# Kernel tuning notes

Measured on AMD Instinct MI355X. Metric: run time of the kernel, lower is better.

Reference implementation:

```python
import jax, jax.numpy as jnp
import numpy as np

BS, P, D, C, ND, K, NC, H = 32, 196, 512, 100, 51, 50, 800, 8
LAMBDA, BETA, EPS = 0.5, 5.5, 1e-5


def _ln(x, g, b):
    m = x.mean(-1, keepdims=True)
    v = jnp.mean((x - m) ** 2, axis=-1, keepdims=True)
    return (x - m) / jnp.sqrt(v + EPS) * g + b


def _norm(x):
    return x / jnp.linalg.norm(x, axis=-1, keepdims=True)


def _bonder(x, kv, Wq, Wk, Wv, Wo, ln1_g, ln1_b, ln2_g, ln2_b, W1, b1, W2, b2):
    # cross-attn block: queries = text prompts [B,N,d], kv = retrieved patch feats [B,M,d]
    B, N, d = x.shape
    M = kv.shape[1]
    dh = d // H
    q = (_ln(x, ln1_g, ln1_b) @ Wq).reshape(B, N, H, dh)
    k = (kv @ Wk).reshape(B, M, H, dh)
    v = (kv @ Wv).reshape(B, M, H, dh)
    att = jax.nn.softmax(jnp.einsum('bnhd,bmhd->bhnm', q, k) / np.sqrt(dh).astype(np.float32), axis=-1)
    o = jnp.einsum('bhnm,bmhd->bnhd', att, v).reshape(B, N, d) @ Wo
    x = x + o
    h = _ln(x, ln2_g, ln2_b)
    return x + jax.nn.gelu(h @ W1 + b1) @ W2 + b2


def _dense_logits(gfeat, local, all_text, mean_text, topk):
    # gfeat [b,d], local [b,p,d], all_text [C,n,d], mean_text [C,d]
    base = gfeat @ mean_text.T                                   # [b,C]
    w = jnp.einsum('bd,bpd->bp', gfeat, local)                   # [b,p]
    atf = jnp.transpose(all_text, (1, 0, 2))                     # [n,C,d]
    v = jax.nn.softmax(jnp.einsum('cd,ncd->nc', mean_text, atf), axis=0)  # [n,C]
    sim = jnp.einsum('bpd,ncd->bcpn', local, atf)                # [b,C,p,n]
    vals, idx = jax.lax.top_k(jnp.transpose(sim, (0, 1, 3, 2)), topk)     # over patch dim
    sim_topk = jnp.transpose(vals, (0, 1, 3, 2))                 # [b,C,k,n]
    idx = jnp.transpose(idx, (0, 1, 3, 2))                       # [b,C,k,n]
    idx_w = idx[:, 0, :, 0]                                      # [b,k]
    w_topk = jax.nn.softmax(jnp.take_along_axis(w, idx_w, axis=1), axis=-1)  # [b,k]
    weight = jnp.einsum('bk,nc->bckn', w_topk, v)                # [b,C,k,n]
    return base + jnp.sum(sim_topk * weight, axis=(-2, -1))


def setup_inputs() -> dict:
    key = jax.random.key(0)
    ks = jax.random.split(key, 12)
    s = 0.02
    labels = jax.random.randint(ks[10], (BS,), 0, C)
    cache_labels = jax.random.randint(ks[11], (NC,), 0, C)
    return {
        'local_feat': jax.random.normal(ks[0], (BS, P, D)),
        'Wa': jnp.eye(D) + s * jax.random.normal(ks[1], (D, D)),
        'text_cache': jax.random.normal(ks[2], (C, ND, D)),
        'Wq': s * jax.random.normal(ks[3], (D, D)),
        'Wk': s * jax.random.normal(ks[4], (D, D)),
        'Wv': s * jax.random.normal(ks[5], (D, D)),
        'Wo': s * jax.random.normal(ks[6], (D, D)),
        'ln1_g': jnp.ones((D,)), 'ln1_b': jnp.zeros((D,)),
        'ln2_g': jnp.ones((D,)), 'ln2_b': jnp.zeros((D,)),
        'W1': s * jax.random.normal(ks[7], (D, 4 * D)), 'b1': jnp.zeros((4 * D,)),
        'W2': s * jax.random.normal(ks[8], (4 * D, D)), 'b2': jnp.zeros((D,)),
        'logit_scale': jnp.asarray(np.log(1.0 / 0.07), jnp.float32),
        'ensemble_scale': jnp.asarray(-2.0, jnp.float32),
        'raw_cache_local_feats': jax.random.normal(ks[9], (NC, P, D)),
        'cache_values': jax.nn.one_hot(cache_labels, C, dtype=jnp.float32),
        'labels': labels,
        'cache_labels': cache_labels,
    }


def reference(local_feat, Wa, text_cache, Wq, Wk, Wv, Wo, ln1_g, ln1_b, ln2_g, ln2_b,
              W1, b1, W2, b2, logit_scale, ensemble_scale, raw_cache_local_feats,
              cache_values, labels, cache_labels):
    bs = local_feat.shape[0]
    adapted_local = _norm(local_feat @ Wa.T)                      # [b,p,d]
    adapted_global = _norm(adapted_local.mean(axis=1))            # [b,d]
    base_text_mean = _norm(jax.lax.stop_gradient(text_cache).mean(axis=1))  # [C,d]
    sim_to_text = jax.lax.stop_gradient(adapted_local @ base_text_mean.T)   # [b,p,C]
    sim_target = sim_to_text[jnp.arange(bs), :, labels]           # [b,p]
    topk_idx = jax.lax.top_k(sim_target, K)[1]
    botk_idx = jax.lax.top_k(-sim_target, K)[1]
    topk_feats = jnp.take_along_axis(adapted_local, topk_idx[:, :, None], axis=1)  # [b,K,d]
    botk_feats = jnp.take_along_axis(adapted_local, botk_idx[:, :, None], axis=1)
    # training branch: bonder on ground-truth class prompts, scatter into bias_full
    l2p = text_cache[labels]                                      # [b,ND,d]
    text_bias = _bonder(l2p, jax.lax.stop_gradient(topk_feats),
                        Wq, Wk, Wv, Wo, ln1_g, ln1_b, ln2_g, ln2_b, W1, b1, W2, b2)
    bias_full = jnp.zeros((bs, C, ND, D), local_feat.dtype).at[jnp.arange(bs), labels].set(text_bias)
    bias_avg = bias_full.mean(axis=0)                             # [C,ND,d]
    refined = text_cache + LAMBDA * bias_avg
    refined_norm = _norm(refined)
    refined_mean_norm = _norm(refined_norm.mean(axis=1))
    ls = jnp.exp(logit_scale)
    inter = ls * _dense_logits(adapted_global, adapted_local, refined_norm, refined_mean_norm, K)
    # tip-adapter cache branch
    cache_adapted = _norm(raw_cache_local_feats @ Wa.T)           # [Nc,p,d]
    cache_sim = jax.lax.stop_gradient(cache_adapted @ base_text_mean.T)
    cache_sim_target = cache_sim[jnp.arange(cache_sim.shape[0]), :, cache_labels]
    cache_topk_idx = jax.lax.top_k(cache_sim_target, K)[1]
    cache_topk_feats = jnp.take_along_axis(cache_adapted, cache_topk_idx[:, :, None], axis=1)
    cache_keys = _norm(cache_topk_feats.mean(axis=1))             # [Nc,d]
    query_keys = _norm(topk_feats.mean(axis=1))                   # [b,d]
    affinity = jnp.exp(-BETA * (1.0 - query_keys @ cache_keys.T))
    intra = affinity @ cache_values                               # [b,C]
    scale = jax.nn.sigmoid(ensemble_scale)
    logits = inter * (1 - scale) + intra * ls * scale
    return (logits, inter, intra, adapted_global, topk_feats, botk_feats, refined_norm)
```

## Files before the change

kernel.cpp:

```cpp
#include <hip/hip_runtime.h>
#include <math.h>

#define DEV static __device__ __forceinline__

typedef __attribute__((ext_vector_type(8))) short short8v;
typedef __attribute__((ext_vector_type(8))) _Float16 half8v;
typedef __attribute__((ext_vector_type(4))) float f32x4;

DEV unsigned encf(float f){ unsigned b=__float_as_uint(f); return b ^ (0x80000000u | (unsigned)((int)b>>31)); }
DEV unsigned long long pkvi(float v, int idx){
  return ((unsigned long long)encf(v)<<32) | (unsigned long long)(0xffffffffu - (unsigned)idx);
}
DEV unsigned long long wave_max_ull(unsigned long long u){
  #pragma unroll
  for (int m=1;m<64;m<<=1){ unsigned long long o = __shfl_xor(u, m); if (o>u) u=o; }
  return u;
}
DEV float wave_sum(float v){
  #pragma unroll
  for (int m=32;m;m>>=1) v += __shfl_xor(v, m);
  return v;
}
DEV float blk_sum256(float v, float* scr){
  v = wave_sum(v);
  __syncthreads();
  if ((threadIdx.x & 63)==0) scr[threadIdx.x>>6] = v;
  __syncthreads();
  return scr[0]+scr[1]+scr[2]+scr[3];
}
DEV float gelu_f(float x){ return 0.5f*x*(1.f + tanhf(0.7978845608028654f*(x + 0.044715f*x*x*x))); }
DEV unsigned short f2bf(float x){
  unsigned u = __float_as_uint(x);
  unsigned r = (u + 0x7fffu + ((u>>16)&1u)) >> 16;
  return (unsigned short)r;
}
DEV float bf2f(unsigned short h){ return __uint_as_float(((unsigned)h)<<16); }
DEV void gld16(const void* g, void* l){
  __builtin_amdgcn_global_load_lds((const __attribute__((address_space(1))) unsigned int*)g,
                                   (__attribute__((address_space(3))) unsigned int*)l, 16, 0, 0);
}
template<int CTRL>
DEV float dppf(float x){
  return __int_as_float(__builtin_amdgcn_mov_dpp(__float_as_int(x), CTRL, 0xF, 0xF, false));
}

template<bool TRANS, bool SUBI>
__global__ __launch_bounds__(256) void k_convw(const float* __restrict__ W,
    unsigned short* __restrict__ hi, unsigned short* __restrict__ lo, int R, int C){
  int n = blockIdx.x;
  int K = TRANS ? R : C;
  for (int k = threadIdx.x; k < K; k += 256){
    float x = TRANS ? W[(size_t)k*C + n] : W[(size_t)n*C + k];
    if (SUBI && k==n) x -= 1.f;
    unsigned short h = f2bf(x);
    hi[(size_t)n*K + k] = h;
    if (lo) lo[(size_t)n*K + k] = f2bf(x - bf2f(h));
  }
}

__global__ __launch_bounds__(256) void k_convw4(
  const float* __restrict__ Wq, const float* __restrict__ Wk,
  const float* __restrict__ Wv, const float* __restrict__ Wo,
  unsigned short* __restrict__ qh, unsigned short* __restrict__ ql,
  unsigned short* __restrict__ kh, unsigned short* __restrict__ kl,
  unsigned short* __restrict__ vh, unsigned short* __restrict__ vl,
  unsigned short* __restrict__ oh, unsigned short* __restrict__ ol)
{
  int n = blockIdx.x;
  const float* W; unsigned short *hi, *lo;
  switch(blockIdx.y){
    case 0: W=Wq; hi=qh; lo=ql; break;
    case 1: W=Wk; hi=kh; lo=kl; break;
    case 2: W=Wv; hi=vh; lo=vl; break;
    default: W=Wo; hi=oh; lo=ol; break;
  }
  for (int k = threadIdx.x; k < 512; k += 256){
    float x = W[(size_t)k*512 + n];
    unsigned short h = f2bf(x);
    hi[(size_t)n*512 + k] = h;
    lo[(size_t)n*512 + k] = f2bf(x - bf2f(h));
  }
}

__global__ __launch_bounds__(256) void k_convd2(const float* __restrict__ Wa, unsigned short* __restrict__ Dfrag){
  int e = blockIdx.x;
  int tile = e>>4, lr = e&15;
  for (int d = threadIdx.x; d < 512; d += 256){
    float x = Wa[(size_t)e*512 + d] - (e==d ? 1.f : 0.f);
    union { _Float16 hh; unsigned short u; } cv;
    cv.hh = (_Float16)x;
    int ks = d>>5, q = (d>>3)&3, el = d&7;
    Dfrag[(size_t)(((tile*16+ks)*64 + q*16 + lr)*8 + el)] = cv.u;
  }
}

template<int EPI>
__global__ __launch_bounds__(256,2) void gemmAB(
  const unsigned short* __restrict__ Ahi, const unsigned short* __restrict__ Alo,
  const unsigned short* __restrict__ Bhi, const unsigned short* __restrict__ Blo,
  float* __restrict__ Cp, unsigned short* __restrict__ Chi, unsigned short* __restrict__ Clo,
  const int M, const int N, const int K,
  const float* __restrict__ bias, const float* __restrict__ resid)
{
  __shared__ __align__(16) char sm[32768];
  const int t = threadIdx.x, lane = t&63, wid = t>>6;
  const int row0 = blockIdx.x*128, col0 = blockIdx.y*128;
  f32x4 acc[2][8];
  #pragma unroll
  for (int i=0;i<2;++i)
    #pragma unroll
    for (int j=0;j<8;++j) acc[i][j] = (f32x4){0.f,0.f,0.f,0.f};

  int offA[2], offB[8];
  #pragma unroll
  for (int mt=0; mt<2; ++mt){
    int row = (2*wid+mt)*16 + (lane&15);
    int sp = (lane>>4) ^ ((row>>1)&3);
    offA[mt] = row*64 + sp*16;
  }
  #pragma unroll
  for (int nt=0; nt<8; ++nt){
    int row = nt*16 + (lane&15);
    int sp = (lane>>4) ^ ((row>>1)&3);
    offB[nt] = row*64 + sp*16;
  }

  const int nks = K >> 5;
  for (int ks=0; ks<nks; ++ks){
    #pragma unroll
    for (int i=0;i<2;++i){
      int s = i*256 + t, row = s>>2, sl2 = s&3, slog = sl2 ^ ((row>>1)&3);
      size_t ga = (size_t)(row0+row)*K + ks*32 + slog*8;
      size_t gb = (size_t)(col0+row)*K + ks*32 + slog*8;
      int dst = (i*256 + wid*64)*16;
      gld16(Ahi + ga, sm + dst);
      gld16(Alo + ga, sm + 8192 + dst);
      gld16(Bhi + gb, sm + 16384 + dst);
      gld16(Blo + gb, sm + 24576 + dst);
    }
    __syncthreads();
    short8v ah0 = *(short8v*)(sm + offA[0]);
    short8v ah1 = *(short8v*)(sm + offA[1]);
    short8v al0 = *(short8v*)(sm + 8192 + offA[0]);
    short8v al1 = *(short8v*)(sm + 8192 + offA[1]);
    #pragma unroll
    for (int nt=0; nt<8; ++nt){
      short8v bh = *(short8v*)(sm + 16384 + offB[nt]);
      short8v bl = *(short8v*)(sm + 24576 + offB[nt]);
      acc[0][nt] = __builtin_amdgcn_mfma_f32_16x16x32_bf16(ah0, bh, acc[0][nt], 0,0,0);
      acc[0][nt] = __builtin_amdgcn_mfma_f32_16x16x32_bf16(ah0, bl, acc[0][nt], 0,0,0);
      acc[0][nt] = __builtin_amdgcn_mfma_f32_16x16x32_bf16(al0, bh, acc[0][nt], 0,0,0);
      acc[1][nt] = __builtin_amdgcn_mfma_f32_16x16x32_bf16(ah1, bh, acc[1][nt], 0,0,0);
      acc[1][nt] = __builtin_amdgcn_mfma_f32_16x16x32_bf16(ah1, bl, acc[1][nt], 0,0,0);
      acc[1][nt] = __builtin_amdgcn_mfma_f32_16x16x32_bf16(al1, bh, acc[1][nt], 0,0,0);
    }
    __syncthreads();
  }

  #pragma unroll
  for (int mt=0; mt<2; ++mt){
    #pragma unroll
    for (int nt=0; nt<8; ++nt){
      int n = col0 + nt*16 + (lane&15);
      int mb = row0 + (2*wid+mt)*16 + (lane>>4)*4;
      #pragma unroll
      for (int j=0;j<4;++j){
        int m = mb + j;
        if (m < M){
          float v = acc[mt][nt][j];
          if (EPI & 1) v += bias[n];
          if (EPI & 2) v = gelu_f(v);
          if (EPI & 4) v += resid[(size_t)m*N + n];
          if (EPI & 8){
            unsigned short h = f2bf(v);
            Chi[(size_t)m*N + n] = h;
            Clo[(size_t)m*N + n] = f2bf(v - bf2f(h));
          } else {
            Cp[(size_t)m*N + n] = v;
          }
        }
      }
    }
  }
}

__global__ __launch_bounds__(256,2) void gemmABQKV(
  const unsigned short* __restrict__ lnH, const unsigned short* __restrict__ lnL,
  const unsigned short* __restrict__ tkH, const unsigned short* __restrict__ tkL,
  const unsigned short* __restrict__ qh, const unsigned short* __restrict__ ql,
  const unsigned short* __restrict__ kh, const unsigned short* __restrict__ kl,
  const unsigned short* __restrict__ vh, const unsigned short* __restrict__ vl,
  float* __restrict__ qb, float* __restrict__ kb, float* __restrict__ vbuf)
{
  __shared__ __align__(16) char sm[32768];
  const int z = blockIdx.z;
  const unsigned short* Ahi = (z==0)? lnH : tkH;
  const unsigned short* Alo = (z==0)? lnL : tkL;
  const unsigned short* Bhi = (z==0)? qh : (z==1? kh : vh);
  const unsigned short* Blo = (z==0)? ql : (z==1? kl : vl);
  float* Cp = (z==0)? qb : (z==1? kb : vbuf);
  const int M = (z==0)? 1632 : 1600;
  const int K = 512, N = 512;
  const int t = threadIdx.x, lane = t&63, wid = t>>6;
  const int row0 = blockIdx.x*128, col0 = blockIdx.y*128;
  f32x4 acc[2][8];
  #pragma unroll
  for (int i=0;i<2;++i)
    #pragma unroll
    for (int j=0;j<8;++j) acc[i][j] = (f32x4){0.f,0.f,0.f,0.f};

  int offA[2], offB[8];
  #pragma unroll
  for (int mt=0; mt<2; ++mt){
    int row = (2*wid+mt)*16 + (lane&15);
    int sp = (lane>>4) ^ ((row>>1)&3);
    offA[mt] = row*64 + sp*16;
  }
  #pragma unroll
  for (int nt=0; nt<8; ++nt){
    int row = nt*16 + (lane&15);
    int sp = (lane>>4) ^ ((row>>1)&3);
    offB[nt] = row*64 + sp*16;
  }

  for (int ks=0; ks<16; ++ks){
    #pragma unroll
    for (int i=0;i<2;++i){
      int s = i*256 + t, row = s>>2, sl2 = s&3, slog = sl2 ^ ((row>>1)&3);
      size_t ga = (size_t)(row0+row)*K + ks*32 + slog*8;
      size_t gb = (size_t)(col0+row)*K + ks*32 + slog*8;
      int dst = (i*256 + wid*64)*16;
      gld16(Ahi + ga, sm + dst);
      gld16(Alo + ga, sm + 8192 + dst);
      gld16(Bhi + gb, sm + 16384 + dst);
      gld16(Blo + gb, sm + 24576 + dst);
    }
    __syncthreads();
    short8v ah0 = *(short8v*)(sm + offA[0]);
    short8v ah1 = *(short8v*)(sm + offA[1]);
    short8v al0 = *(short8v*)(sm + 8192 + offA[0]);
    short8v al1 = *(short8v*)(sm + 8192 + offA[1]);
    #pragma unroll
    for (int nt=0; nt<8; ++nt){
      short8v bh = *(short8v*)(sm + 16384 + offB[nt]);
      short8v bl = *(short8v*)(sm + 24576 + offB[nt]);
      acc[0][nt] = __builtin_amdgcn_mfma_f32_16x16x32_bf16(ah0, bh, acc[0][nt], 0,0,0);
      acc[0][nt] = __builtin_amdgcn_mfma_f32_16x16x32_bf16(ah0, bl, acc[0][nt], 0,0,0);
      acc[0][nt] = __builtin_amdgcn_mfma_f32_16x16x32_bf16(al0, bh, acc[0][nt], 0,0,0);
      acc[1][nt] = __builtin_amdgcn_mfma_f32_16x16x32_bf16(ah1, bh, acc[1][nt], 0,0,0);
      acc[1][nt] = __builtin_amdgcn_mfma_f32_16x16x32_bf16(ah1, bl, acc[1][nt], 0,0,0);
      acc[1][nt] = __builtin_amdgcn_mfma_f32_16x16x32_bf16(al1, bh, acc[1][nt], 0,0,0);
    }
    __syncthreads();
  }

  #pragma unroll
  for (int mt=0; mt<2; ++mt){
    #pragma unroll
    for (int nt=0; nt<8; ++nt){
      int n = col0 + nt*16 + (lane&15);
      int mb = row0 + (2*wid+mt)*16 + (lane>>4)*4;
      #pragma unroll
      for (int j=0;j<4;++j){
        int m = mb + j;
        if (m < M) Cp[(size_t)m*N + n] = acc[mt][nt][j];
      }
    }
  }
}

__global__ __launch_bounds__(512,1) void k_un7(
  const float* __restrict__ raw, const unsigned short* __restrict__ Dfrag,
  const float* __restrict__ zm, const int* __restrict__ clab,
  float* __restrict__ cdot, float* __restrict__ norm2)
{
  __shared__ __align__(16) char Alds[131072];
  __shared__ float n2sq[128];
  __shared__ float n2x[4][128];
  const int t = threadIdx.x, lane = t&63;
  const int wid = t>>6, wm = wid>>2, wn = wid&3;
  const int m0 = blockIdx.x*128;

  {
    const int row = t>>2, sl = t&3;
    const int slg = sl ^ ((row>>1)&3);
    const float* rp = raw + ((size_t)(m0+row))*512 + slg*8;
    const float* zp = zm + (size_t)clab[(m0+row)/196]*512 + slg*8;
    float sq=0.f, cd=0.f;
    #pragma unroll
    for (int c4=0; c4<4; ++c4){
      float4 pr[8], pz[8];
      #pragma unroll
      for (int i=0;i<4;++i){
        pr[2*i]   = *(const float4*)(rp + (c4*4+i)*32);
        pr[2*i+1] = *(const float4*)(rp + (c4*4+i)*32 + 4);
      }
      #pragma unroll
      for (int i=0;i<4;++i){
        pz[2*i]   = *(const float4*)(zp + (c4*4+i)*32);
        pz[2*i+1] = *(const float4*)(zp + (c4*4+i)*32 + 4);
      }
      #pragma unroll
      for (int i=0;i<4;++i){
        int ks = c4*4+i;
        float xs[8] = {pr[2*i].x,pr[2*i].y,pr[2*i].z,pr[2*i].w,
                       pr[2*i+1].x,pr[2*i+1].y,pr[2*i+1].z,pr[2*i+1].w};
        float zs[8] = {pz[2*i].x,pz[2*i].y,pz[2*i].z,pz[2*i].w,
                       pz[2*i+1].x,pz[2*i+1].y,pz[2*i+1].z,pz[2*i+1].w};
        union { _Float16 h[8]; f32x4 f; } uh;
        #pragma unroll
        for (int u=0;u<8;++u){
          uh.h[u] = (_Float16)xs[u];
          sq = fmaf(xs[u],xs[u],sq);
          cd = fmaf(xs[u],zs[u],cd);
        }
        *(f32x4*)(Alds + ks*8192 + t*16) = uh.f;
      }
    }
    sq += __shfl_xor(sq,1); sq += __shfl_xor(sq,2);
    cd += __shfl_xor(cd,1); cd += __shfl_xor(cd,2);
    if (sl==0){ n2sq[row] = sq; cdot[m0+row] = cd; }
  }
  __syncthreads();

  int offA[4];
  #pragma unroll
  for (int mt=0; mt<4; ++mt){
    int row = wm*64 + mt*16 + (lane&15);
    int sp = (lane>>4) ^ ((row>>1)&3);
    offA[mt] = row*64 + sp*16;
  }
  const half8v* Dv = (const half8v*)Dfrag;

  float pacc[4][4];
  #pragma unroll
  for (int a_=0;a_<4;++a_)
    #pragma unroll
    for (int b_=0;b_<4;++b_) pacc[a_][b_]=0.f;

  for (int eb2=0; eb2<4; ++eb2){
    f32x4 acc[4][2];
    #pragma unroll
    for (int a_=0;a_<4;++a_)
      #pragma unroll
      for (int b_=0;b_<2;++b_) acc[a_][b_] = (f32x4){0.f,0.f,0.f,0.f};

    #pragma unroll 4
    for (int ks=0; ks<16; ++ks){
      half8v af[4], bf[2];
      #pragma unroll
      for (int mt=0; mt<4; ++mt) af[mt] = *(half8v*)(Alds + ks*8192 + offA[mt]);
      #pragma unroll
      for (int nt=0; nt<2; ++nt) bf[nt] = Dv[(size_t)(((eb2*8 + wn*2 + nt)*16 + ks)*64 + lane)];
      #pragma unroll
      for (int mt=0; mt<4; ++mt)
        #pragma unroll
        for (int nt=0; nt<2; ++nt)
          acc[mt][nt] = __builtin_amdgcn_mfma_f32_16x16x32_f16(af[mt], bf[nt], acc[mt][nt], 0,0,0);
    }

    #pragma unroll
    for (int mt=0; mt<4; ++mt){
      #pragma unroll
      for (int j=0;j<4;++j){
        int row = wm*64 + mt*16 + (lane>>4)*4 + j;
        float p = 0.f;
        #pragma unroll
        for (int nt=0; nt<2; ++nt){
          float U = acc[mt][nt][j];
          int eg = eb2*128 + wn*32 + nt*16 + (lane&15);
          int kse = eg>>5, o = eg&31;
          int sll = (o>>3) ^ ((row>>1)&3);
          float rh = (float)*(const _Float16*)(Alds + kse*8192 + row*64 + sll*16 + (o&7)*2);
          p = fmaf(U, 2.f*rh + U, p);
        }
        p += __shfl_xor(p,1); p += __shfl_xor(p,2); p += __shfl_xor(p,4); p += __shfl_xor(p,8);
        pacc[mt][j] += p;
      }
    }
  }

  __syncthreads();
  if ((lane&15)==0){
    #pragma unroll
    for (int mt=0; mt<4; ++mt)
      #pragma unroll
      for (int j=0;j<4;++j)
        n2x[wn][wm*64 + mt*16 + (lane>>4)*4 + j] = pacc[mt][j];
  }
  __syncthreads();
  if (t < 128)
    norm2[m0+t] = n2sq[t] + n2x[0][t] + n2x[1][t] + n2x[2][t] + n2x[3][t];
}

__global__ __launch_bounds__(256) void k_rownorm(const float* __restrict__ in, float* __restrict__ out,
                                                 unsigned short* __restrict__ bfo, int nrows){
  __shared__ float scr[4];
  int r = blockIdx.x, t = threadIdx.x; (void)nrows;
  const float* p = in + (size_t)r*512;
  float x0 = p[t], x1 = p[t+256];
  float ss = blk_sum256(x0*x0 + x1*x1, scr);
  float inv = 1.f/sqrtf(ss);
  float v0 = x0*inv, v1 = x1*inv;
  out[(size_t)r*512 + t] = v0;
  out[(size_t)r*512 + t + 256] = v1;
  if (bfo){
    size_t br = (size_t)(r/196)*256 + (r%196);
    bfo[br*512 + t]     = f2bf(v0);
    bfo[br*512 + t+256] = f2bf(v1);
  }
}

__global__ __launch_bounds__(256) void k_meanrows_norm(const float* __restrict__ in, int nper,
                                                       float* __restrict__ o1, float* __restrict__ o2){
  __shared__ float scr[4];
  int g = blockIdx.x, t = threadIdx.x;
  float s0=0.f, s1=0.f;
  const float* bp = in + (size_t)g*nper*512;
  for (int r=0;r<nper;++r){ s0 += bp[(size_t)r*512+t]; s1 += bp[(size_t)r*512+t+256]; }
  float ss = blk_sum256(s0*s0+s1*s1, scr);
  float inv = 1.f/sqrtf(ss);
  float v0 = s0*inv, v1 = s1*inv;
  o1[(size_t)g*512+t]=v0; o1[(size_t)g*512+t+256]=v1;
  if (o2){ o2[(size_t)g*512+t]=v0; o2[(size_t)g*512+t+256]=v1; }
}

__global__ __launch_bounds__(256) void k_zmat(const float* __restrict__ btm, const float* __restrict__ Wa, float* __restrict__ z){
  int c = blockIdx.x, t = threadIdx.x;
  float a0=0.f, a1=0.f;
  for (int d=0; d<512; ++d){
    float bv = btm[c*512+d];
    a0 = fmaf(bv, Wa[(size_t)d*512+t], a0);
    a1 = fmaf(bv, Wa[(size_t)d*512+t+256], a1);
  }
  z[c*512+t]=a0; z[c*512+t+256]=a1;
}

__global__ __launch_bounds__(256) void k_dot_bp(const float* __restrict__ AL, const float* __restrict__ vecs,
                                                const int* __restrict__ sel, float* __restrict__ outv, int mode){
  int wid = blockIdx.x*4 + (threadIdx.x>>6);
  int lane = threadIdx.x & 63;
  int b = wid/196;
  int vrow = sel ? sel[b] : (mode ? 0 : b);
  const float* a = AL + (size_t)wid*512 + lane*8;
  const float* v = vecs + (size_t)vrow*512 + lane*8;
  float4 a0 = *(const float4*)a, a1 = *(const float4*)(a+4);
  float4 v0 = *(const float4*)v, v1 = *(const float4*)(v+4);
  float s = a0.x*v0.x + a0.y*v0.y + a0.z*v0.z + a0.w*v0.w
          + a1.x*v1.x + a1.y*v1.y + a1.z*v1.z + a1.w*v1.w;
  s = wave_sum(s);
  if (lane==0) outv[wid] = s;
}

__global__ __launch_bounds__(256) void k_dot2(const float* __restrict__ AL, const float* __restrict__ AGw,
                                              const float* __restrict__ RN00,
                                              float* __restrict__ wbp, float* __restrict__ sLw){
  int wid = blockIdx.x*4 + (threadIdx.x>>6);
  int lane = threadIdx.x & 63;
  int b = wid/196;
  const float* a = AL + (size_t)wid*512 + lane*8;
  const float* v = AGw + (size_t)b*512 + lane*8;
  const float* w = RN00 + lane*8;
  float4 a0=*(const float4*)a, a1=*(const float4*)(a+4);
  float4 v0=*(const float4*)v, v1=*(const float4*)(v+4);
  float4 w0=*(const float4*)w, w1=*(const float4*)(w+4);
  float s1 = a0.x*v0.x+a0.y*v0.y+a0.z*v0.z+a0.w*v0.w + a1.x*v1.x+a1.y*v1.y+a1.z*v1.z+a1.w*v1.w;
  float s2 = a0.x*w0.x+a0.y*w0.y+a0.z*w0.z+a0.w*w0.w + a1.x*w1.x+a1.y*w1.y+a1.z*w1.z+a1.w*w1.w;
  s1 = wave_sum(s1); s2 = wave_sum(s2);
  if (lane==0){ wbp[wid] = s1; sLw[wid] = s2; }
}

__global__ __launch_bounds__(64) void k_topbot(const float* __restrict__ st, int* __restrict__ tki, int* __restrict__ bki){
  int b = blockIdx.x, lane = threadIdx.x;
  float v[4];
  #pragma unroll
  for (int s2=0;s2<4;++s2){ int p = lane + 64*s2; v[s2] = (p<196)? st[b*196+p] : -INFINITY; }
  for (int k=0;k<50;++k){
    unsigned long long best = pkvi(v[0], lane);
    { unsigned long long cc=pkvi(v[1],lane+64);  if(cc>best)best=cc; }
    { unsigned long long cc=pkvi(v[2],lane+128); if(cc>best)best=cc; }
    { unsigned long long cc=pkvi(v[3],lane+192); if(cc>best)best=cc; }
    best = wave_max_ull(best);
    int widx = (int)(0xffffffffu - (unsigned)(best & 0xffffffffu));
    if (lane==0) tki[b*50+k] = widx;
    if ((widx & 63)==lane) v[widx>>6] = -INFINITY;
  }
  #pragma unroll
  for (int s2=0;s2<4;++s2){ int p = lane + 64*s2; v[s2] = (p<196)? -st[b*196+p] : -INFINITY; }
  for (int k=0;k<50;++k){
    unsigned long long best = pkvi(v[0], lane);
    { unsigned long long cc=pkvi(v[1],lane+64);  if(cc>best)best=cc; }
    { unsigned long long cc=pkvi(v[2],lane+128); if(cc>best)best=cc; }
    { unsigned long long cc=pkvi(v[3],lane+192); if(cc>best)best=cc; }
    best = wave_max_ull(best);
    int widx = (int)(0xffffffffu - (unsigned)(best & 0xffffffffu));
    if (lane==0) bki[b*50+k] = widx;
    if ((widx & 63)==lane) v[widx>>6] = -INFINITY;
  }
}

__global__ __launch_bounds__(256) void k_gather_tb(const float* __restrict__ AL, const int* __restrict__ tki, const int* __restrict__ bki,
                                                   float* __restrict__ otk, float* __restrict__ obk, float* __restrict__ qk,
                                                   unsigned short* __restrict__ tkH, unsigned short* __restrict__ tkL){
  __shared__ float scr[4];
  int b = blockIdx.x, t = threadIdx.x;
  float a0=0.f, a1=0.f;
  for (int k=0;k<50;++k){
    int pt = tki[b*50+k];
    const float* rp = AL + ((size_t)b*196+pt)*512;
    float x0 = rp[t], x1 = rp[t+256];
    size_t ro = ((size_t)b*50+k)*512;
    otk[ro + t] = x0; otk[ro + t+256] = x1;
    unsigned short h0 = f2bf(x0), h1 = f2bf(x1);
    tkH[ro + t] = h0;      tkL[ro + t]     = f2bf(x0 - bf2f(h0));
    tkH[ro + t+256] = h1;  tkL[ro + t+256] = f2bf(x1 - bf2f(h1));
    a0 += x0; a1 += x1;
    int pb = bki[b*50+k];
    const float* rb = AL + ((size_t)b*196+pb)*512;
    obk[ro + t] = rb[t]; obk[ro + t+256] = rb[t+256];
  }
  float ss = blk_sum256(a0*a0+a1*a1, scr);
  float inv = 1.f/sqrtf(ss);
  qk[b*512+t] = a0*inv; qk[b*512+t+256] = a1*inv;
}

__global__ __launch_bounds__(256) void k_gxln(const float* __restrict__ tc, const int* __restrict__ labels,
                                              const float* __restrict__ g, const float* __restrict__ be,
                                              float* __restrict__ xb,
                                              unsigned short* __restrict__ hi, unsigned short* __restrict__ lo){
  __shared__ float scr[4];
  int r = blockIdx.x, t = threadIdx.x;
  int b = r/51, n = r%51;
  int lab = labels[b];
  const float* src = tc + ((size_t)lab*51 + n)*512;
  float x0 = src[t], x1 = src[t+256];
  xb[(size_t)r*512+t] = x0; xb[(size_t)r*512+t+256] = x1;
  float s = blk_sum256(x0+x1, scr);
  float mean = s*(1.f/512.f);
  float ss = blk_sum256(x0*x0+x1*x1, scr);
  float var = ss*(1.f/512.f) - mean*mean;
  float inv = 1.f/sqrtf(var + 1e-5f);
  float v0 = (x0-mean)*inv*g[t]     + be[t];
  float v1 = (x1-mean)*inv*g[t+256] + be[t+256];
  unsigned short h0 = f2bf(v0), h1 = f2bf(v1);
  hi[(size_t)r*512+t]     = h0;  lo[(size_t)r*512+t]     = f2bf(v0 - bf2f(h0));
  hi[(size_t)r*512+t+256] = h1;  lo[(size_t)r*512+t+256] = f2bf(v1 - bf2f(h1));
}

__global__ __launch_bounds__(256) void k_layernorm2(const float* __restrict__ in,
                                                    unsigned short* __restrict__ hi, unsigned short* __restrict__ lo,
                                                    const float* __restrict__ g, const float* __restrict__ be){
  __shared__ float scr[4];
  int r = blockIdx.x, t = threadIdx.x;
  const float* p = in + (size_t)r*512;
  float x0=p[t], x1=p[t+256];
  float s = blk_sum256(x0+x1, scr);
  float mean = s*(1.f/512.f);
  float ss = blk_sum256(x0*x0+x1*x1, scr);
  float var = ss*(1.f/512.f) - mean*mean;
  float inv = 1.f/sqrtf(var + 1e-5f);
  float v0 = (x0-mean)*inv*g[t]     + be[t];
  float v1 = (x1-mean)*inv*g[t+256] + be[t+256];
  unsigned short h0 = f2bf(v0), h1 = f2bf(v1);
  hi[(size_t)r*512+t]     = h0;  lo[(size_t)r*512+t]     = f2bf(v0 - bf2f(h0));
  hi[(size_t)r*512+t+256] = h1;  lo[(size_t)r*512+t+256] = f2bf(v1 - bf2f(h1));
}

__global__ __launch_bounds__(256) void k_attn2(const float* __restrict__ qb, const float* __restrict__ kb,
                                               const float* __restrict__ vb,
                                               unsigned short* __restrict__ obH, unsigned short* __restrict__ obL){
  int b = blockIdx.x, h = blockIdx.y, t = threadIdx.x;
  __shared__ float qh[51][65];
  __shared__ float kh[50][65];
  __shared__ float vh[50][65];
  __shared__ float S[51][52];
  for (int f=t; f<51*64; f+=256){ int n=f>>6, d=f&63; qh[n][d] = qb[((size_t)(b*51+n))*512 + h*64 + d]; }
  for (int f=t; f<50*64; f+=256){ int m=f>>6, d=f&63;
    kh[m][d] = kb[((size_t)(b*50+m))*512 + h*64 + d];
    vh[m][d] = vb[((size_t)(b*50+m))*512 + h*64 + d];
  }
  __syncthreads();
  for (int f=t; f<51*50; f+=256){
    int n=f/50, m=f%50;
    float s=0.f;
    #pragma unroll 8
    for (int d=0; d<64; ++d) s = fmaf(qh[n][d], kh[m][d], s);
    S[n][m] = s*0.125f;
  }
  __syncthreads();
  int w = t>>6, lane = t&63;
  for (int n=w; n<51; n+=4){
    float x = (lane<50)? S[n][lane] : -INFINITY;
    float mx = x;
    #pragma unroll
    for (int m2=32;m2;m2>>=1) mx = fmaxf(mx, __shfl_xor(mx,m2));
    float e = (lane<50)? expf(x-mx) : 0.f;
    float se = wave_sum(e);
    if (lane<50) S[n][lane] = e/se;
  }
  __syncthreads();
  for (int f=t; f<51*64; f+=256){
    int n=f>>6, d=f&63;
    float s=0.f;
    #pragma unroll 10
    for (int m=0;m<50;++m) s = fmaf(S[n][m], vh[m][d], s);
    size_t idx = ((size_t)(b*51+n))*512 + h*64 + d;
    unsigned short hh = f2bf(s);
    obH[idx] = hh; obL[idx] = f2bf(s - bf2f(hh));
  }
}

__global__ __launch_bounds__(256) void k_refined(const float* __restrict__ tc, const float* __restrict__ TB,
                                                 const int* __restrict__ labels, float* __restrict__ RN,
                                                 unsigned short* __restrict__ RNbf){
  __shared__ float scr[4];
  __shared__ int labL[32];
  int blk = blockIdx.x, t = threadIdx.x;
  int c = blk/51, n = blk%51;
  if (t<32) labL[t] = labels[t];
  __syncthreads();
  float r0=0.f, r1=0.f;
  for (int b=0;b<32;++b){
    if (labL[b]==c){
      const float* tb = TB + ((size_t)(b*51+n))*512;
      r0 += tb[t]; r1 += tb[t+256];
    }
  }
  const float* tcp = tc + ((size_t)(c*51+n))*512;
  r0 = tcp[t]     + r0*(1.f/64.f);
  r1 = tcp[t+256] + r1*(1.f/64.f);
  float ss = blk_sum256(r0*r0+r1*r1, scr);
  float inv = 1.f/sqrtf(ss);
  float v0 = r0*inv, v1 = r1*inv;
  RN[((size_t)(c*51+n))*512+t]     = v0;
  RN[((size_t)(c*51+n))*512+t+256] = v1;
  size_t br = (size_t)c*64 + n;
  RNbf[br*512 + t]     = f2bf(v0);
  RNbf[br*512 + t+256] = f2bf(v1);
}

__global__ __launch_bounds__(256) void k_vsm(const float* __restrict__ RN, const float* __restrict__ RMN, float* __restrict__ vsm){
  __shared__ float sv[51];
  int c = blockIdx.x, t = threadIdx.x, w = t>>6, lane = t&63;
  for (int n=w; n<51; n+=4){
    const float* a = RN + ((size_t)(c*51+n))*512 + lane*8;
    const float* m = RMN + (size_t)c*512 + lane*8;
    float4 a0=*(const float4*)a, a1=*(const float4*)(a+4);
    float4 m0=*(const float4*)m, m1=*(const float4*)(m+4);
    float s = a0.x*m0.x+a0.y*m0.y+a0.z*m0.z+a0.w*m0.w + a1.x*m1.x+a1.y*m1.y+a1.z*m1.z+a1.w*m1.w;
    s = wave_sum(s);
    if (lane==0) sv[n]=s;
  }
  __syncthreads();
  if (t<64){
    float x = (t<51)? sv[t] : -INFINITY;
    float mx = x;
    #pragma unroll
    for (int m2=32;m2;m2>>=1) mx = fmaxf(mx, __shfl_xor(mx,m2));
    float e = (t<51)? expf(x-mx) : 0.f;
    float se = wave_sum(e);
    if (t<51) vsm[c*51+t] = e/se;
  }
}

__global__ __launch_bounds__(64) void k_wtopk(const float* __restrict__ sLg,
                                              const float* __restrict__ wbp, float* __restrict__ wtk){
  __shared__ int idxL[50];
  int b = blockIdx.x, lane = threadIdx.x;
  float v[4];
  #pragma unroll
  for (int s2=0;s2<4;++s2){ int p = lane+64*s2; v[s2] = (p<196)? sLg[b*196+p] : -INFINITY; }
  for (int k=0;k<50;++k){
    unsigned long long best = pkvi(v[0], lane);
    { unsigned long long cc=pkvi(v[1],lane+64);  if(cc>best)best=cc; }
    { unsigned long long cc=pkvi(v[2],lane+128); if(cc>best)best=cc; }
    { unsigned long long cc=pkvi(v[3],lane+192); if(cc>best)best=cc; }
    best = wave_max_ull(best);
    int widx = (int)(0xffffffffu - (unsigned)(best & 0xffffffffu));
    if (lane==0) idxL[k]=widx;
    if ((widx&63)==lane) v[widx>>6] = -INFINITY;
  }
  __syncthreads();
  float wv = (lane<50)? wbp[b*196 + idxL[lane]] : -INFINITY;
  float mx = wv;
  #pragma unroll
  for (int m2=32;m2;m2>>=1) mx = fmaxf(mx, __shfl_xor(mx,m2));
  float e = (lane<50)? expf(wv-mx) : 0.f;
  float se = wave_sum(e);
  if (lane<50) wtk[b*50+lane] = e/se;
}

__global__ __launch_bounds__(256,3) void k_dense3(
  const unsigned short* __restrict__ ALbf, const unsigned short* __restrict__ RNbf,
  const float* __restrict__ RMN, const float* __restrict__ AG,
  const float* __restrict__ vsm, const float* __restrict__ wtk,
  const float* __restrict__ lsp, float* __restrict__ interw)
{
  __shared__ __align__(16) char smem[52224];
  __shared__ float red[8];
  __shared__ float wtkS[52];
  const int c = blockIdx.x, b = blockIdx.y;
  const int t = threadIdx.x, lane = t&63, wid = t>>6;

  if (t<50) wtkS[t] = wtk[b*50+t];
  if (t<64){
    const float* a = AG + (size_t)b*512 + t*8;
    const float* m = RMN + (size_t)c*512 + t*8;
    float4 a0=*(const float4*)a, a1=*(const float4*)(a+4);
    float4 m0=*(const float4*)m, m1=*(const float4*)(m+4);
    float s = a0.x*m0.x+a0.y*m0.y+a0.z*m0.z+a0.w*m0.w + a1.x*m1.x+a1.y*m1.y+a1.z*m1.z+a1.w*m1.w;
    s = wave_sum(s);
    if (t==0) red[4] = s;
  }

  f32x4 acc[4][4];
  #pragma unroll
  for (int i=0;i<4;++i)
    #pragma unroll
    for (int j=0;j<4;++j) acc[i][j] = (f32x4){0.f,0.f,0.f,0.f};

  int offA[4], offB[4];
  #pragma unroll
  for (int mt=0; mt<4; ++mt){
    int row = wid*64 + mt*16 + (lane&15);
    int sp = (lane>>4) ^ ((row>>1)&3);
    offA[mt] = row*64 + sp*16;
  }
  #pragma unroll
  for (int nt=0; nt<4; ++nt){
    int row = nt*16 + (lane&15);
    int sp = (lane>>4) ^ ((row>>1)&3);
    offB[nt] = row*64 + sp*16;
  }

  const unsigned short* Abase = ALbf + ((size_t)b<<17);
  const unsigned short* Bbase = RNbf + ((size_t)c<<15);

  auto STAGE = [&](int buf, int ks){
    const int Ab = buf? 20480 : 0, Bb = buf? 36864 : 16384;
    #pragma unroll
    for (int i=0;i<4;++i){
      int q = i*256 + t;
      int row = q>>2, sl = q&3;
      int slog = sl ^ ((row>>1)&3);
      gld16(Abase + ((size_t)row<<9) + ks*32 + slog*8, smem + Ab + (i*256 + wid*64)*16);
    }
    {
      int row = t>>2, sl = t&3;
      int slog = sl ^ ((row>>1)&3);
      gld16(Bbase + ((size_t)row<<9) + ks*32 + slog*8, smem + Bb + (wid*64)*16);
    }
  };

  STAGE(0, 0);
  __syncthreads();
  for (int ks=0; ks<16; ++ks){
    const int cur = ks&1;
    if (ks<15) STAGE(cur^1, ks+1);
    const int Ab = cur? 20480 : 0, Bb = cur? 36864 : 16384;
    short8v af[4], bf[4];
    #pragma unroll
    for (int mt=0; mt<4; ++mt) af[mt] = *(short8v*)(smem + Ab + offA[mt]);
    #pragma unroll
    for (int nt=0; nt<4; ++nt) bf[nt] = *(short8v*)(smem + Bb + offB[nt]);
    #pragma unroll
    for (int mt=0; mt<4; ++mt)
      #pragma unroll
      for (int nt=0; nt<4; ++nt)
        acc[mt][nt] = __builtin_amdgcn_mfma_f32_16x16x32_bf16(af[mt], bf[nt], acc[mt][nt], 0,0,0);
    __syncthreads();
  }

  #pragma unroll
  for (int mt=0; mt<4; ++mt){
    #pragma unroll
    for (int nt=0; nt<4; ++nt){
      int n = nt*16 + (lane&15);
      if (n < 51){
        int p0 = wid*64 + mt*16 + (lane>>4)*4;
        int addr = ((n<<10) + (p0<<2)) ^ ((((n&7)^wid)&7)<<4);
        *(f32x4*)(smem + addr) = acc[mt][nt];
      }
    }
  }
  __syncthreads();

  const int n = wid*16 + (lane>>2);
  const int q = lane&3;
  float v[64];
  if (n < 51){
    #pragma unroll
    for (int i=0;i<16;++i){
      int p = q*64 + i*4;
      int addr = ((n<<10) + (p<<2)) ^ ((((n&7)^q)&7)<<4);
      *(f32x4*)&v[i*4] = *(f32x4*)(smem + addr);
    }
  } else {
    #pragma unroll
    for (int i=0;i<64;++i) v[i] = -INFINITY;
  }
  if (q==3){
    #pragma unroll
    for (int j=4;j<64;++j) v[j] = -INFINITY;
  }

  #pragma unroll
  for (int k=2;k<=64;k<<=1){
    #pragma unroll
    for (int j=k>>1;j>=1;j>>=1){
      #pragma unroll
      for (int i=0;i<64;++i){
        if ((i&j)==0){
          int p2 = i|j;
          float a=v[i], bb=v[p2];
          if ((i&k)!=0){ v[i]=fminf(a,bb); v[p2]=fmaxf(a,bb); }
          else         { v[i]=fmaxf(a,bb); v[p2]=fminf(a,bb); }
        }
      }
    }
  }
  #pragma unroll
  for (int i=0;i<32;++i){
    float pa = dppf<0xB1>(v[63-i]);
    float pb = dppf<0xB1>(v[i]);
    v[i]    = fmaxf(v[i], pa);
    v[63-i] = fmaxf(v[63-i], pb);
  }
  #pragma unroll
  for (int j=32;j>=1;j>>=1){
    #pragma unroll
    for (int i=0;i<64;++i){
      if ((i&j)==0){ int p2=i|j; float a=v[i],bb=v[p2]; v[i]=fmaxf(a,bb); v[p2]=fminf(a,bb); }
    }
  }
  #pragma unroll
  for (int i=0;i<32;++i){
    float pa = dppf<0x4E>(v[63-i]);
    float pb = dppf<0x4E>(v[i]);
    v[i]    = fmaxf(v[i], pa);
    v[63-i] = fmaxf(v[63-i], pb);
  }
  #pragma unroll
  for (int j=32;j>=1;j>>=1){
    #pragma unroll
    for (int i=0;i<64;++i){
      if ((i&j)==0){ int p2=i|j; float a=v[i],bb=v[p2]; v[i]=fmaxf(a,bb); v[p2]=fminf(a,bb); }
    }
  }

  float s = 0.f;
  #pragma unroll
  for (int r=0;r<50;++r) s = fmaf(wtkS[r], v[r], s);
  float val = (q==0 && n<51) ? vsm[c*51+n]*s : 0.f;
  val = wave_sum(val);
  if (lane==0) red[wid] = val;
  __syncthreads();
  if (t==0){
    float ls = expf(lsp[0]);
    interw[b*100+c] = ls*(red[4] + red[0]+red[1]+red[2]+red[3]);
  }
}

__global__ __launch_bounds__(256) void k_cache_sel(const float* __restrict__ cdot, const float* __restrict__ norm2,
                                                   const float* __restrict__ raw,
                                                   unsigned short* __restrict__ rbH, unsigned short* __restrict__ rbL){
  __shared__ int idxL[50];
  __shared__ float invL[50];
  int i = blockIdx.x, t = threadIdx.x;
  if (t < 64){
    int lane = t;
    float v[4];
    #pragma unroll
    for (int s2=0;s2<4;++s2){
      int p = lane+64*s2;
      v[s2] = (p<196)? cdot[(size_t)i*196+p] * (1.f/sqrtf(norm2[(size_t)i*196+p])) : -INFINITY;
    }
    for (int k=0;k<50;++k){
      unsigned long long best = pkvi(v[0], lane);
      { unsigned long long cc=pkvi(v[1],lane+64);  if(cc>best)best=cc; }
      { unsigned long long cc=pkvi(v[2],lane+128); if(cc>best)best=cc; }
      { unsigned long long cc=pkvi(v[3],lane+192); if(cc>best)best=cc; }
      best = wave_max_ull(best);
      int widx = (int)(0xffffffffu - (unsigned)(best & 0xffffffffu));
      if (lane==0){ idxL[k]=widx; invL[k] = 1.f/sqrtf(norm2[(size_t)i*196+widx]); }
      if ((widx&63)==lane) v[widx>>6] = -INFINITY;
    }
  }
  __syncthreads();
  float a0=0.f, a1=0.f;
  #pragma unroll
  for (int kc=0; kc<5; ++kc){
    float x0[10], x1[10];
    #pragma unroll
    for (int j=0;j<10;++j){
      const float* rp = raw + ((size_t)i*196 + idxL[kc*10+j])*512;
      x0[j] = rp[t]; x1[j] = rp[t+256];
    }
    #pragma unroll
    for (int j=0;j<10;++j){
      float iv = invL[kc*10+j];
      a0 = fmaf(x0[j], iv, a0);
      a1 = fmaf(x1[j], iv, a1);
    }
  }
  unsigned short h0 = f2bf(a0), h1 = f2bf(a1);
  rbH[(size_t)i*512+t]     = h0;  rbL[(size_t)i*512+t]     = f2bf(a0 - bf2f(h0));
  rbH[(size_t)i*512+t+256] = h1;  rbL[(size_t)i*512+t+256] = f2bf(a1 - bf2f(h1));
}

__global__ __launch_bounds__(256) void k_aff(const float* __restrict__ qk, const float* __restrict__ ck, float* __restrict__ aff){
  int gid = blockIdx.x*4 + (threadIdx.x>>6);
  int lane = threadIdx.x&63;
  int b = gid/800, i = gid%800;
  const float* a = qk + (size_t)b*512 + lane*8;
  const float* v = ck + (size_t)i*512 + lane*8;
  float4 a0=*(const float4*)a, a1=*(const float4*)(a+4);
  float4 v0=*(const float4*)v, v1=*(const float4*)(v+4);
  float s = a0.x*v0.x+a0.y*v0.y+a0.z*v0.z+a0.w*v0.w + a1.x*v1.x+a1.y*v1.y+a1.z*v1.z+a1.w*v1.w;
  s = wave_sum(s);
  if (lane==0) aff[gid] = expf(-5.5f*(1.f - s));
}

__global__ __launch_bounds__(128) void k_intra(const float* __restrict__ aff, const float* __restrict__ cv, float* __restrict__ intra){
  __shared__ float affL[800];
  int b = blockIdx.x, t = threadIdx.x;
  for (int f=t; f<800; f+=128) affL[f] = aff[b*800+f];
  __syncthreads();
  if (t<100){
    float s=0.f;
    for (int i=0;i<800;++i) s = fmaf(affL[i], cv[(size_t)i*100+t], s);
    intra[b*100+t]=s;
  }
}

__global__ void k_final(const float* __restrict__ interw, const float* __restrict__ intraw,
                        const float* __restrict__ lsp, const float* __restrict__ esp, float* __restrict__ outp){
  int idx = blockIdx.x*256 + threadIdx.x;
  if (idx < 3200){
    float ls = expf(lsp[0]);
    float sc = 1.f/(1.f + expf(-esp[0]));
    float iv = interw[idx], ia = intraw[idx];
    outp[idx]        = iv*(1.f-sc) + ia*ls*sc;
    outp[3200+idx]   = iv;
    outp[6400+idx]   = ia;
  }
}

extern "C" void kernel_launch(void* const* d_in, const int* in_sizes, int n_in,
                              void* d_out, int out_size, void* d_ws, size_t ws_size,
                              hipStream_t stream)
{
  (void)in_sizes; (void)n_in; (void)out_size; (void)ws_size;
  const float* lf   = (const float*)d_in[0];
  const float* Wa   = (const float*)d_in[1];
  const float* tc   = (const float*)d_in[2];
  const float* Wq   = (const float*)d_in[3];
  const float* Wk   = (const float*)d_in[4];
  const float* Wv   = (const float*)d_in[5];
  const float* Wo   = (const float*)d_in[6];
  const float* ln1g = (const float*)d_in[7];
  const float* ln1b = (const float*)d_in[8];
  const float* ln2g = (const float*)d_in[9];
  const float* ln2b = (const float*)d_in[10];
  const float* W1   = (const float*)d_in[11];
  const float* b1   = (const float*)d_in[12];
  const float* W2   = (const float*)d_in[13];
  const float* b2   = (const float*)d_in[14];
  const float* lsp  = (const float*)d_in[15];
  const float* esp  = (const float*)d_in[16];
  const float* raw  = (const float*)d_in[17];
  const float* cv   = (const float*)d_in[18];
  const int* labels = (const int*)d_in[19];
  const int* clab   = (const int*)d_in[20];

  float* out = (float*)d_out;
  float* outAG = out + 9600;
  float* outTK = out + 25984;
  float* outBK = out + 845184;
  float* outRN = out + 1664384;

  float* wsf = (float*)d_ws;
  size_t o = 0;
  #define WALLOC(name, n) float* name = wsf + o; o += (size_t)(n);
  WALLOC(AL,    6272*512)
  WALLOC(xb,    1632*512)
  WALLOC(qb,    1632*512)
  WALLOC(kb,    1600*512)
  WALLOC(vbuf,  1600*512)
  WALLOC(x2,    1632*512)
  WALLOC(TB,    1632*512)
  WALLOC(btm,   100*512)
  WALLOC(zm,    100*512)
  WALLOC(RMN,   100*512)
  WALLOC(vsm,   5100)
  WALLOC(st,    6272)
  WALLOC(wbp,   6272)
  WALLOC(sLw,   6272)
  WALLOC(AGw,   32*512)
  WALLOC(qkb,   32*512)
  WALLOC(wtk,   1600)
  WALLOC(norm2, 156800)
  WALLOC(cdot,  156800)
  WALLOC(mbuf,  800*512)
  WALLOC(ckb,   800*512)
  WALLOC(aff,   25600)
  WALLOC(interw,3200)
  WALLOC(intraw,3200)
  #undef WALLOC
  int* tki = (int*)(wsf + o); o += 1600;
  int* bki = (int*)(wsf + o); o += 1600;
  unsigned short* ALbf = (unsigned short*)(wsf + o); o += (size_t)32*256*512/2;
  unsigned short* RNbf = (unsigned short*)(wsf + o); o += (size_t)100*64*512/2;
  #define WALLOC16(name, n) unsigned short* name = (unsigned short*)(wsf + o); o += ((size_t)(n)+1)/2;
  WALLOC16(waHi, 262144)  WALLOC16(waLo, 262144)
  WALLOC16(wqHi, 262144)  WALLOC16(wqLo, 262144)
  WALLOC16(wkHi, 262144)  WALLOC16(wkLo, 262144)
  WALLOC16(wvHi, 262144)  WALLOC16(wvLo, 262144)
  WALLOC16(woHi, 262144)  WALLOC16(woLo, 262144)
  WALLOC16(w1Hi, 1048576) WALLOC16(w1Lo, 1048576)
  WALLOC16(w2Hi, 1048576) WALLOC16(w2Lo, 1048576)
  WALLOC16(dfrag, 262144)
  WALLOC16(ln1H, 851968)  WALLOC16(ln1L, 851968)
  WALLOC16(h2H,  851968)  WALLOC16(h2L,  851968)
  WALLOC16(obH,  851968)  WALLOC16(obL,  851968)
  WALLOC16(tkH,  851968)  WALLOC16(tkL,  851968)
  WALLOC16(y1H,  3407872) WALLOC16(y1L,  3407872)
  WALLOC16(rbH,  458752)  WALLOC16(rbL,  458752)
  WALLOC16(lfH,  3211264) WALLOC16(lfL,  3211264)
  #undef WALLOC16

  k_convw<false,false><<<dim3(512), dim3(256), 0, stream>>>(Wa, waHi, waLo, 512,512);
  k_convw4<<<dim3(512,4), dim3(256), 0, stream>>>(Wq,Wk,Wv,Wo, wqHi,wqLo, wkHi,wkLo, wvHi,wvLo, woHi,woLo);
  k_convw<true ,false><<<dim3(2048), dim3(256), 0, stream>>>(W1, w1Hi, w1Lo, 512,2048);
  k_convw<true ,false><<<dim3(512), dim3(256), 0, stream>>>(W2, w2Hi, w2Lo, 2048,512);
  k_convd2<<<dim3(512), dim3(256), 0, stream>>>(Wa, dfrag);
  k_convw<false,false><<<dim3(6272), dim3(256), 0, stream>>>(lf, lfH, lfL, 6272,512);

  hipMemsetAsync(ALbf, 0, ((size_t)32*256*512 + (size_t)100*64*512)*2, stream);

  gemmAB<0><<<dim3(49,4), dim3(256), 0, stream>>>(lfH, lfL, waHi, waLo, AL, nullptr, nullptr, 6272,512,512, nullptr, nullptr);
  k_rownorm<<<dim3(6272), dim3(256), 0, stream>>>(AL, AL, ALbf, 6272);
  k_meanrows_norm<<<dim3(32), dim3(256), 0, stream>>>(AL, 196, AGw, outAG);
  k_meanrows_norm<<<dim3(100), dim3(256), 0, stream>>>(tc, 51, btm, (float*)nullptr);
  k_zmat<<<dim3(100), dim3(256), 0, stream>>>(btm, Wa, zm);
  k_dot_bp<<<dim3(1568), dim3(256), 0, stream>>>(AL, btm, labels, st, 0);
  k_topbot<<<dim3(32), dim3(64), 0, stream>>>(st, tki, bki);
  k_gather_tb<<<dim3(32), dim3(256), 0, stream>>>(AL, tki, bki, outTK, outBK, qkb, tkH, tkL);
  k_gxln<<<dim3(1632), dim3(256), 0, stream>>>(tc, labels, ln1g, ln1b, xb, ln1H, ln1L);
  gemmABQKV<<<dim3(13,4,3), dim3(256), 0, stream>>>(ln1H,ln1L, tkH,tkL, wqHi,wqLo, wkHi,wkLo, wvHi,wvLo, qb, kb, vbuf);
  k_attn2<<<dim3(32,8), dim3(256), 0, stream>>>(qb, kb, vbuf, obH, obL);
  gemmAB<4><<<dim3(13,4), dim3(256), 0, stream>>>(obH, obL, woHi, woLo, x2, nullptr, nullptr, 1632,512,512, nullptr, xb);
  k_layernorm2<<<dim3(1632), dim3(256), 0, stream>>>(x2, h2H, h2L, ln2g, ln2b);
  gemmAB<11><<<dim3(13,16), dim3(256), 0, stream>>>(h2H, h2L, w1Hi, w1Lo, nullptr, y1H, y1L, 1632,2048,512, b1, nullptr);
  gemmAB<5><<<dim3(13,4), dim3(256), 0, stream>>>(y1H, y1L, w2Hi, w2Lo, TB, nullptr, nullptr, 1632,512,2048, b2, x2);
  k_refined<<<dim3(5100), dim3(256), 0, stream>>>(tc, TB, labels, outRN, RNbf);
  k_meanrows_norm<<<dim3(100), dim3(256), 0, stream>>>(outRN, 51, RMN, (float*)nullptr);
  k_vsm<<<dim3(100), dim3(256), 0, stream>>>(outRN, RMN, vsm);
  k_dot2<<<dim3(1568), dim3(256), 0, stream>>>(AL, AGw, outRN, wbp, sLw);
  k_wtopk<<<dim3(32), dim3(64), 0, stream>>>(sLw, wbp, wtk);
  k_dense3<<<dim3(100,32), dim3(256), 0, stream>>>(ALbf, RNbf, RMN, AGw, vsm, wtk, lsp, interw);
  k_un7<<<dim3(1225), dim3(512), 0, stream>>>(raw, dfrag, zm, clab, cdot, norm2);
  k_cache_sel<<<dim3(800), dim3(256), 0, stream>>>(cdot, norm2, raw, rbH, rbL);
  gemmAB<0><<<dim3(7,4), dim3(256), 0, stream>>>(rbH, rbL, waHi, waLo, mbuf, nullptr, nullptr, 800,512,512, nullptr, nullptr);
  k_rownorm<<<dim3(800), dim3(256), 0, stream>>>(mbuf, ckb, (unsigned short*)nullptr, 800);
  k_aff<<<dim3(6400), dim3(256), 0, stream>>>(qkb, ckb, aff);
  k_intra<<<dim3(32), dim3(128), 0, stream>>>(aff, cv, intraw);
  k_final<<<dim3(13), dim3(256), 0, stream>>>(interw, intraw, lsp, esp, out);
}
```

Baseline: 1.013 ms.

## Interleave raw-feature loading with MFMA k-steps in cache adapter kernel

Restructures k_un7 so the fp32 to fp16 staging of raw cache features into LDS is interleaved with the MFMA loop per k-slice. Global loads run two slices ahead, and all four output column blocks accumulate at once (32 accumulators), instead of staging the whole tile and then looping over column blocks. The goal is to overlap global-load latency with tensor math and to read each A fragment from LDS once rather than four times. In exchange it adds a __syncthreads per k-step and much higher register pressure (128 accumulator floats plus prefetch buffers), which could cause spills.

```diff
diff --git a/kernel.cpp b/kernel.cpp
--- a/kernel.cpp
+++ b/kernel.cpp
@@ -281,56 +281,79 @@
   const int wid = t>>6, wm = wid>>2, wn = wid&3;
   const int m0 = blockIdx.x*128;
 
-  {
-    const int row = t>>2, sl = t&3;
-    const int slg = sl ^ ((row>>1)&3);
-    const float* rp = raw + ((size_t)(m0+row))*512 + slg*8;
-    const float* zp = zm + (size_t)clab[(m0+row)/196]*512 + slg*8;
-    float sq=0.f, cd=0.f;
-    #pragma unroll
-    for (int c4=0; c4<4; ++c4){
-      float4 pr[8], pz[8];
+  const int row = t>>2, sl = t&3;
+  const int slg = sl ^ ((row>>1)&3);
+  const float* rp = raw + ((size_t)(m0+row))*512 + slg*8;
+  const float* zp = zm + (size_t)clab[(m0+row)/196]*512 + slg*8;
+
+  int offA[4];
+  #pragma unroll
+  for (int mt=0; mt<4; ++mt){
+    int r2 = wm*64 + mt*16 + (lane&15);
+    int sp = (lane>>4) ^ ((r2>>1)&3);
+    offA[mt] = r2*64 + sp*16;
+  }
+  const half8v* Dv = (const half8v*)Dfrag;
+
+  f32x4 acc[4][4][2];
+  #pragma unroll
+  for (int eb=0;eb<4;++eb)
+    #pragma unroll
+    for (int mt=0;mt<4;++mt)
       #pragma unroll
-      for (int i=0;i<4;++i){
-        pr[2*i]   = *(const float4*)(rp + (c4*4+i)*32);
-        pr[2*i+1] = *(const float4*)(rp + (c4*4+i)*32 + 4);
+      for (int nt=0;nt<2;++nt) acc[eb][mt][nt] = (f32x4){0.f,0.f,0.f,0.f};
+
+  float sq=0.f, cd=0.f;
+  float4 lr[16][2], lz[16][2];
+  #pragma unroll
+  for (int k0=0;k0<2;++k0){
+    lr[k0][0] = *(const float4*)(rp + k0*32);
+    lr[k0][1] = *(const float4*)(rp + k0*32 + 4);
+    lz[k0][0] = *(const float4*)(zp + k0*32);
+    lz[k0][1] = *(const float4*)(zp + k0*32 + 4);
+  }
+
+  #pragma unroll
+  for (int ks=0; ks<16; ++ks){
+    if (ks+2 < 16){
+      lr[ks+2][0] = *(const float4*)(rp + (ks+2)*32);
+      lr[ks+2][1] = *(const float4*)(rp + (ks+2)*32 + 4);
+      lz[ks+2][0] = *(const float4*)(zp + (ks+2)*32);
+      lz[ks+2][1] = *(const float4*)(zp + (ks+2)*32 + 4);
+    }
+    {
+      float xs[8] = {lr[ks][0].x,lr[ks][0].y,lr[ks][0].z,lr[ks][0].w,
+                     lr[ks][1].x,lr[ks][1].y,lr[ks][1].z,lr[ks][1].w};
+      float zs[8] = {lz[ks][0].x,lz[ks][0].y,lz[ks][0].z,lz[ks][0].w,
+                     lz[ks][1].x,lz[ks][1].y,lz[ks][1].z,lz[ks][1].w};
+      union { _Float16 h[8]; f32x4 f; } uh;
+      #pragma unroll
+      for (int u=0;u<8;++u){
+        uh.h[u] = (_Float16)xs[u];
+        sq = fmaf(xs[u],xs[u],sq);
+        cd = fmaf(xs[u],zs[u],cd);
       }
+      *(f32x4*)(Alds + ks*8192 + t*16) = uh.f;
+    }
+    __syncthreads();
+    half8v af[4];
+    #pragma unroll
+    for (int mt=0; mt<4; ++mt) af[mt] = *(half8v*)(Alds + ks*8192 + offA[mt]);
+    #pragma unroll
+    for (int eb=0;eb<4;++eb){
       #pragma unroll
-      for (int i=0;i<4;++i){
-        pz[2*i]   = *(const float4*)(zp + (c4*4+i)*32);
-        pz[2*i+1] = *(const float4*)(zp + (c4*4+i)*32 + 4);
+      for (int nt=0;nt<2;++nt){
+        half8v bf = Dv[(size_t)(((eb*8 + wn*2 + nt)*16 + ks)*64 + lane)];
+        #pragma unroll
+        for (int mt=0;mt<4;++mt)
+          acc[eb][mt][nt] = __builtin_amdgcn_mfma_f32_16x16x32_f16(af[mt], bf, acc[eb][mt][nt], 0,0,0);
       }
-      #pragma unroll
-      for (int i=0;i<4;++i){
-        int ks = c4*4+i;
-        float xs[8] = {pr[2*i].x,pr[2*i].y,pr[2*i].z,pr[2*i].w,
-                       pr[2*i+1].x,pr[2*i+1].y,pr[2*i+1].z,pr[2*i+1].w};
-        float zs[8] = {pz[2*i].x,pz[2*i].y,pz[2*i].z,pz[2*i].w,
-                       pz[2*i+1].x,pz[2*i+1].y,pz[2*i+1].z,pz[2*i+1].w};
-        union { _Float16 h[8]; f32x4 f; } uh;
-        #pragma unroll
-        for (int u=0;u<8;++u){
-          uh.h[u] = (_Float16)xs[u];
-          sq = fmaf(xs[u],xs[u],sq);
-          cd = fmaf(xs[u],zs[u],cd);
-        }
-        *(f32x4*)(Alds + ks*8192 + t*16) = uh.f;
-      }
-    }
-    sq += __shfl_xor(sq,1); sq += __shfl_xor(sq,2);
-    cd += __shfl_xor(cd,1); cd += __shfl_xor(cd,2);
-    if (sl==0){ n2sq[row] = sq; cdot[m0+row] = cd; }
-  }
-  __syncthreads();
-
-  int offA[4];
-  #pragma unroll
-  for (int mt=0; mt<4; ++mt){
-    int row = wm*64 + mt*16 + (lane&15);
-    int sp = (lane>>4) ^ ((row>>1)&3);
-    offA[mt] = row*64 + sp*16;
-  }
-  const half8v* Dv = (const half8v*)Dfrag;
+    }
+  }
+
+  sq += __shfl_xor(sq,1); sq += __shfl_xor(sq,2);
+  cd += __shfl_xor(cd,1); cd += __shfl_xor(cd,2);
+  if (sl==0){ n2sq[row] = sq; cdot[m0+row] = cd; }
 
   float pacc[4][4];
   #pragma unroll
@@ -338,40 +361,21 @@
     #pragma unroll
     for (int b_=0;b_<4;++b_) pacc[a_][b_]=0.f;
 
-  for (int eb2=0; eb2<4; ++eb2){
-    f32x4 acc[4][2];
-    #pragma unroll
-    for (int a_=0;a_<4;++a_)
-      #pragma unroll
-      for (int b_=0;b_<2;++b_) acc[a_][b_] = (f32x4){0.f,0.f,0.f,0.f};
-
-    #pragma unroll 4
-    for (int ks=0; ks<16; ++ks){
-      half8v af[4], bf[2];
-      #pragma unroll
-      for (int mt=0; mt<4; ++mt) af[mt] = *(half8v*)(Alds + ks*8192 + offA[mt]);
-      #pragma unroll
-      for (int nt=0; nt<2; ++nt) bf[nt] = Dv[(size_t)(((eb2*8 + wn*2 + nt)*16 + ks)*64 + lane)];
-      #pragma unroll
-      for (int mt=0; mt<4; ++mt)
-        #pragma unroll
-        for (int nt=0; nt<2; ++nt)
-          acc[mt][nt] = __builtin_amdgcn_mfma_f32_16x16x32_f16(af[mt], bf[nt], acc[mt][nt], 0,0,0);
-    }
-
+  #pragma unroll
+  for (int eb=0; eb<4; ++eb){
     #pragma unroll
     for (int mt=0; mt<4; ++mt){
       #pragma unroll
       for (int j=0;j<4;++j){
-        int row = wm*64 + mt*16 + (lane>>4)*4 + j;
+        int row2 = wm*64 + mt*16 + (lane>>4)*4 + j;
         float p = 0.f;
         #pragma unroll
         for (int nt=0; nt<2; ++nt){
-          float U = acc[mt][nt][j];
-          int eg = eb2*128 + wn*32 + nt*16 + (lane&15);
+          float U = acc[eb][mt][nt][j];
+          int eg = eb*128 + wn*32 + nt*16 + (lane&15);
           int kse = eg>>5, o = eg&31;
-          int sll = (o>>3) ^ ((row>>1)&3);
-          float rh = (float)*(const _Float16*)(Alds + kse*8192 + row*64 + sll*16 + (o&7)*2);
+          int sll = (o>>3) ^ ((row2>>1)&3);
+          float rh = (float)*(const _Float16*)(Alds + kse*8192 + row2*64 + sll*16 + (o&7)*2);
           p = fmaf(U, 2.f*rh + U, p);
         }
         p += __shfl_xor(p,1); p += __shfl_xor(p,2); p += __shfl_xor(p,4); p += __shfl_xor(p,8);
```

Result: slower. 1.091 ms (+7.7%).
